# Kernel optimization log

Hardware: AMD Instinct MI355X
Metric: run time of the kernel (lower is better)

## Reference

```python
import jax, jax.numpy as jnp
import numpy as np


def setup_inputs() -> dict:
    key = jax.random.key(0)
    x = jax.random.normal(key, (2, 192, 360, 720), dtype=jnp.float32)
    return {"x": x, "pad_width": 3}


def reference(x, pad_width):
    # x: [B, C, H, W]; geo-cyclic padding:
    #  - circular (periodic) padding of width pad_width in longitude (last axis)
    #  - polar wrap: top/bottom halo rows are rows reflected across the pole,
    #    shifted by half the longitude circle (W // 2).
    B, C, H, W = x.shape
    p = pad_width
    # Circular longitude padding: [B, C, H, W + 2p]
    cp = jnp.concatenate([x[:, :, :, -p:], x, x[:, :, :, :p]], axis=3)
    mid = W // 2
    # Each halo row is cat(row[mid:], row[:mid]) == roll by -mid along longitude.
    rolled = jnp.roll(cp, -mid, axis=3)
    i = np.arange(p)
    top_rows = (p - i - 1) % H          # rows written at output rows 0..p-1
    bottom_rows = (H - i - 1) % H       # rows written at output rows H+p..H+2p-1
    top = rolled[:, :, top_rows, :]     # [B, C, p, W+2p]
    bottom = rolled[:, :, bottom_rows, :]
    # Output: [B, C, H + 2p, W + 2p]
    return jnp.concatenate([top, cp, bottom], axis=2)
```

## Files before the change

kernel.cpp:

```cpp
#include <hip/hip_runtime.h>


typedef float f4a __attribute__((ext_vector_type(4), aligned(16)));
typedef float f4u __attribute__((ext_vector_type(4), aligned(4)));

__global__ __launch_bounds__(256) void geo_pad_kernel(const float* __restrict__ x,
                                                      float* __restrict__ out) {
    constexpr int W = 720, H = 360, p = 3, Wp = 726, Hp = 366;
    constexpr unsigned BULK = 384u * 360u * 180u;
    constexpr unsigned EPP  = 360u * 6u + 6u * 726u;

    const unsigned t = blockIdx.x * 256u + threadIdx.x;

    if (t < BULK) {
        const unsigned k  = t % 180u;
        const unsigned rr = t / 180u;
        const unsigned r  = rr % 360u;
        const unsigned bc = rr / 360u;

        const f4a* src = reinterpret_cast<const f4a*>(
            x + (size_t)(bc * 360u + r) * W) + k;
        f4a v = __builtin_nontemporal_load(src);

        float* dst = out + ((size_t)bc * Hp + (r + 3)) * Wp + 3 + 4 * k;
        f4u sv;
        sv.x = v.x; sv.y = v.y; sv.z = v.z; sv.w = v.w;
        __builtin_nontemporal_store(sv, reinterpret_cast<f4u*>(dst));
    } else {
        const unsigned e  = t - BULK;
        const unsigned bc = e / EPP;
        const unsigned q  = e % EPP;

        int ho, col, h, w;
        if (q < 2160u) {
            const int r  = (int)(q / 6u);
            const int c6 = (int)(q % 6u);
            ho  = r + p;
            h   = r;
            col = (c6 < 3) ? c6 : (720 + c6);
            w   = (c6 < 3) ? (717 + c6) : (c6 - 3);
        } else {
            const unsigned q2 = q - 2160u;
            const int hr = (int)(q2 / (unsigned)Wp);
            col = (int)(q2 % (unsigned)Wp);
            ho  = (hr < p) ? hr : (H + hr);
            h   = (hr < p) ? (p - 1 - hr) : (362 - hr);
            int wr = col + W / 2;
            if (wr >= Wp) wr -= Wp;
            w = wr - p;
            if (w < 0) w += W; else if (w >= W) w -= W;
        }
        out[((size_t)bc * Hp + ho) * Wp + col] =
            x[((size_t)bc * H + h) * W + w];
    }
}

extern "C" void kernel_launch(void* const* d_in, const int* in_sizes, int n_in,
                              void* d_out, int out_size, void* d_ws, size_t ws_size,
                              hipStream_t stream) {
    const float* x = (const float*)d_in[0];
    float* out = (float*)d_out;

    const unsigned total = 384u * 360u * 180u + 384u * (360u * 6u + 6u * 726u);
    geo_pad_kernel<<<total / 256u, 256, 0, stream>>>(x, out);
}
```

Measured before the change: 144.0 us.

## Fold halo work into bulk threads and widen edge copies

Removes the separate tail of edge threads. Each bulk thread now also handles halo work: one thread copies three longitude-wrap floats per row side, and polar halo rows are copied two floats at a time, using a float2 load when the source columns are contiguous. The launch shrinks to the bulk thread count. The halo work is unevenly spread across warps, so the threads with low indices do extra work and their branches diverge.

Result: slower. 149.8 us (+4.1%).

```diff
diff --git a/kernel.cpp b/kernel.cpp
--- a/kernel.cpp
+++ b/kernel.cpp
@@ -3,16 +3,18 @@
 
 typedef float f4a __attribute__((ext_vector_type(4), aligned(16)));
 typedef float f4u __attribute__((ext_vector_type(4), aligned(4)));
+typedef float f2u __attribute__((ext_vector_type(2), aligned(4)));
 
 __global__ __launch_bounds__(256) void geo_pad_kernel(const float* __restrict__ x,
                                                       float* __restrict__ out) {
     constexpr int W = 720, H = 360, p = 3, Wp = 726, Hp = 366;
-    constexpr unsigned BULK = 384u * 360u * 180u;
-    constexpr unsigned EPP  = 360u * 6u + 6u * 726u;
+    constexpr unsigned SEG2 = 360u * 384u * 2u;
+    constexpr unsigned SEG1 = 363u * 6u * 384u;
+    constexpr unsigned EDGE = SEG2 + SEG1;
 
     const unsigned t = blockIdx.x * 256u + threadIdx.x;
 
-    if (t < BULK) {
+    {
         const unsigned k  = t % 180u;
         const unsigned rr = t / 180u;
         const unsigned r  = rr % 360u;
@@ -23,35 +25,50 @@
         f4a v = __builtin_nontemporal_load(src);
 
         float* dst = out + ((size_t)bc * Hp + (r + 3)) * Wp + 3 + 4 * k;
-        f4u sv;
-        sv.x = v.x; sv.y = v.y; sv.z = v.z; sv.w = v.w;
+        f4u sv; sv.x = v.x; sv.y = v.y; sv.z = v.z; sv.w = v.w;
         __builtin_nontemporal_store(sv, reinterpret_cast<f4u*>(dst));
-    } else {
-        const unsigned e  = t - BULK;
-        const unsigned bc = e / EPP;
-        const unsigned q  = e % EPP;
+    }
 
-        int ho, col, h, w;
-        if (q < 2160u) {
-            const int r  = (int)(q / 6u);
-            const int c6 = (int)(q % 6u);
-            ho  = r + p;
-            h   = r;
-            col = (c6 < 3) ? c6 : (720 + c6);
-            w   = (c6 < 3) ? (717 + c6) : (c6 - 3);
+    if (t < EDGE) {
+        if (t < SEG2) {
+            const unsigned rowid = t >> 1;
+            const int side = (int)(t & 1u);
+            const unsigned bc = rowid / 360u;
+            const unsigned r  = rowid % 360u;
+            const float* __restrict__ srow = x + (size_t)(bc * 360u + r) * W;
+            float* __restrict__ orow = out + ((size_t)bc * Hp + (r + 3)) * Wp;
+            const int sbase = side ? 0 : 717;
+            const int obase = side ? 723 : 0;
+#pragma unroll
+            for (int i = 0; i < 3; ++i)
+                __builtin_nontemporal_store(srow[sbase + i], &orow[obase + i]);
         } else {
-            const unsigned q2 = q - 2160u;
-            const int hr = (int)(q2 / (unsigned)Wp);
-            col = (int)(q2 % (unsigned)Wp);
-            ho  = (hr < p) ? hr : (H + hr);
-            h   = (hr < p) ? (p - 1 - hr) : (362 - hr);
-            int wr = col + W / 2;
-            if (wr >= Wp) wr -= Wp;
-            w = wr - p;
-            if (w < 0) w += W; else if (w >= W) w -= W;
+            const unsigned e2 = t - SEG2;
+            const unsigned g     = e2 % 363u;
+            const unsigned rowid = e2 / 363u;
+            const unsigned hr = rowid % 6u;
+            const unsigned bc = rowid / 6u;
+            const int ho = (hr < 3u) ? (int)hr : (int)(360u + hr);
+            const int h  = (hr < 3u) ? (int)(2u - hr) : (int)(362u - hr);
+
+            const float* __restrict__ srow = x + (size_t)(bc * 360u + (unsigned)h) * W;
+            float* __restrict__ orow = out + ((size_t)bc * Hp + ho) * Wp;
+
+            const int c0 = 2 * (int)g;
+            int wr0 = c0 + 360;     if (wr0 >= Wp) wr0 -= Wp;
+            int wr1 = c0 + 361;     if (wr1 >= Wp) wr1 -= Wp;
+            int w0 = wr0 - p; if (w0 < 0) w0 += W; else if (w0 >= W) w0 -= W;
+            int w1 = wr1 - p; if (w1 < 0) w1 += W; else if (w1 >= W) w1 -= W;
+
+            f2u sv;
+            if (w1 == w0 + 1) {
+                sv = __builtin_nontemporal_load(
+                    reinterpret_cast<const f2u*>(srow + w0));
+            } else {
+                sv.x = srow[w0]; sv.y = srow[w1];
+            }
+            __builtin_nontemporal_store(sv, reinterpret_cast<f2u*>(orow + c0));
         }
-        out[((size_t)bc * Hp + ho) * Wp + col] =
-            x[((size_t)bc * H + h) * W + w];
     }
 }
 
@@ -61,6 +78,6 @@
     const float* x = (const float*)d_in[0];
     float* out = (float*)d_out;
 
-    const unsigned total = 384u * 360u * 180u + 384u * (360u * 6u + 6u * 726u);
+    const unsigned total = 384u * 360u * 180u;
     geo_pad_kernel<<<total / 256u, 256, 0, stream>>>(x, out);
 }
```

## Interleave edge blocks among bulk blocks and vectorize polar halo rows by pairs

Applied to the files above, without the earlier changes.

Halo (edge) blocks are now spread evenly through the grid instead of all running at the end, so they overlap with the bulk copy rather than forming a slow tail. Polar halo rows are written two floats per thread with 8-byte stores, using a paired load when the source columns are contiguous. This halves the thread count for the polar rows. It costs extra 64-bit division per block to map each block to bulk or edge work.

Result: no change. 142.4 us, median of 2 (-1.1%).

```diff
diff --git a/kernel.cpp b/kernel.cpp
--- a/kernel.cpp
+++ b/kernel.cpp
@@ -3,16 +3,22 @@
 
 typedef float f4a __attribute__((ext_vector_type(4), aligned(16)));
 typedef float f4u __attribute__((ext_vector_type(4), aligned(4)));
+typedef float f2u __attribute__((ext_vector_type(2), aligned(4)));
 
 __global__ __launch_bounds__(256) void geo_pad_kernel(const float* __restrict__ x,
                                                       float* __restrict__ out) {
     constexpr int W = 720, H = 360, p = 3, Wp = 726, Hp = 366;
-    constexpr unsigned BULK = 384u * 360u * 180u;
-    constexpr unsigned EPP  = 360u * 6u + 6u * 726u;
+    constexpr unsigned EPP  = 2160u + 6u * 363u;
+    constexpr unsigned EBLK = 384u * EPP / 256u;
+    constexpr unsigned TBLK = 97200u + EBLK;
 
-    const unsigned t = blockIdx.x * 256u + threadIdx.x;
+    const unsigned i = blockIdx.x;
+    const unsigned long long iE = (unsigned long long)i * EBLK;
+    const unsigned e_before = (unsigned)(iE / TBLK);
+    const unsigned e_after  = (unsigned)((iE + EBLK) / TBLK);
 
-    if (t < BULK) {
+    if (e_after == e_before) {
+        const unsigned t = (i - e_before) * 256u + threadIdx.x;
         const unsigned k  = t % 180u;
         const unsigned rr = t / 180u;
         const unsigned r  = rr % 360u;
@@ -23,35 +29,46 @@
         f4a v = __builtin_nontemporal_load(src);
 
         float* dst = out + ((size_t)bc * Hp + (r + 3)) * Wp + 3 + 4 * k;
-        f4u sv;
-        sv.x = v.x; sv.y = v.y; sv.z = v.z; sv.w = v.w;
+        f4u sv; sv.x = v.x; sv.y = v.y; sv.z = v.z; sv.w = v.w;
         __builtin_nontemporal_store(sv, reinterpret_cast<f4u*>(dst));
     } else {
-        const unsigned e  = t - BULK;
+        const unsigned e = e_before * 256u + threadIdx.x;
         const unsigned bc = e / EPP;
         const unsigned q  = e % EPP;
 
-        int ho, col, h, w;
         if (q < 2160u) {
             const int r  = (int)(q / 6u);
             const int c6 = (int)(q % 6u);
-            ho  = r + p;
-            h   = r;
-            col = (c6 < 3) ? c6 : (720 + c6);
-            w   = (c6 < 3) ? (717 + c6) : (c6 - 3);
+            const int ho  = r + p;
+            const int h   = r;
+            const int col = (c6 < 3) ? c6 : (720 + c6);
+            const int w   = (c6 < 3) ? (717 + c6) : (c6 - 3);
+            out[((size_t)bc * Hp + ho) * Wp + col] =
+                x[((size_t)bc * H + h) * W + w];
         } else {
             const unsigned q2 = q - 2160u;
-            const int hr = (int)(q2 / (unsigned)Wp);
-            col = (int)(q2 % (unsigned)Wp);
-            ho  = (hr < p) ? hr : (H + hr);
-            h   = (hr < p) ? (p - 1 - hr) : (362 - hr);
-            int wr = col + W / 2;
-            if (wr >= Wp) wr -= Wp;
-            w = wr - p;
-            if (w < 0) w += W; else if (w >= W) w -= W;
+            const unsigned g  = q2 % 363u;
+            const int hr = (int)(q2 / 363u);
+            const int ho = (hr < p) ? hr : (H + hr);
+            const int h  = (hr < p) ? (p - 1 - hr) : (362 - hr);
+
+            const float* __restrict__ srow = x + ((size_t)bc * H + h) * W;
+            float* __restrict__ orow = out + ((size_t)bc * Hp + ho) * Wp;
+
+            const int c0 = 2 * (int)g;
+            int wr0 = c0 + 360; if (wr0 >= Wp) wr0 -= Wp;
+            int wr1 = c0 + 361; if (wr1 >= Wp) wr1 -= Wp;
+            int w0 = wr0 - p; if (w0 < 0) w0 += W; else if (w0 >= W) w0 -= W;
+            int w1 = wr1 - p; if (w1 < 0) w1 += W; else if (w1 >= W) w1 -= W;
+
+            f2u sv;
+            if (w1 == w0 + 1) {
+                sv = *reinterpret_cast<const f2u*>(srow + w0);
+            } else {
+                sv.x = srow[w0]; sv.y = srow[w1];
+            }
+            __builtin_nontemporal_store(sv, reinterpret_cast<f2u*>(orow + c0));
         }
-        out[((size_t)bc * Hp + ho) * Wp + col] =
-            x[((size_t)bc * H + h) * W + w];
     }
 }
 
@@ -61,6 +78,5 @@
     const float* x = (const float*)d_in[0];
     float* out = (float*)d_out;
 
-    const unsigned total = 384u * 360u * 180u + 384u * (360u * 6u + 6u * 726u);
-    geo_pad_kernel<<<total / 256u, 256, 0, stream>>>(x, out);
+    geo_pad_kernel<<<103707u, 256, 0, stream>>>(x, out);
 }
```
